# Performance work log

Hardware: AMD Instinct MI355X
Metric: run time of the kernel (lower is better)

The kernel has to match this reference:

```python
import jax, jax.numpy as jnp
import numpy as np

B, N, H, T = 128, 512, 128, 32


def setup_inputs() -> dict:
    key = jax.random.key(0)
    ks = jax.random.split(key, 6)
    s = 0.05  # small init scale keeps softmax logits sane
    return {
        "encoder_outputs": jax.random.normal(ks[0], (B, N, H), jnp.float32),
        "W_ih": jax.random.normal(ks[1], (4 * H, H), jnp.float32) * s,
        "W_hh": jax.random.normal(ks[2], (4 * H, H), jnp.float32) * s,
        "b_ih": jnp.zeros((4 * H,), jnp.float32),
        "b_hh": jnp.zeros((4 * H,), jnp.float32),
        "W1": jax.random.normal(ks[3], (H, H), jnp.float32) * s,
        "W2": jax.random.normal(ks[4], (H, H), jnp.float32) * s,
        "v": jax.random.normal(ks[5], (H,), jnp.float32) * s,
        "decode_steps": T,
    }


def reference(encoder_outputs, W_ih, W_hh, b_ih, b_hh, W1, W2, v, decode_steps):
    b, n, h = encoder_outputs.shape
    dtype = encoder_outputs.dtype
    # W1(encoder_outputs) is loop-invariant: hoist it (same math as the torch loop)
    enc_trans = jnp.einsum("bnh,kh->bnk", encoder_outputs, W1)  # [B,n,H]

    dec0 = encoder_outputs.mean(axis=1)  # [B,H]
    hx0 = jnp.zeros((b, h), dtype)
    cx0 = jnp.zeros((b, h), dtype)
    mask0 = jnp.zeros((b, n), bool)
    key0 = jax.random.key(42)
    rows = jnp.arange(b)

    def step(carry, _):
        dec_input, hx, cx, mask, key = carry
        # torch.nn.LSTMCell: gates ordered i, f, g, o
        gates = dec_input @ W_ih.T + b_ih + hx @ W_hh.T + b_hh  # [B,4H]
        i, f, g, o = jnp.split(gates, 4, axis=-1)
        i = jax.nn.sigmoid(i)
        f = jax.nn.sigmoid(f)
        g = jnp.tanh(g)
        o = jax.nn.sigmoid(o)
        cx_new = f * cx + i * g
        hx_new = o * jnp.tanh(cx_new)
        # additive attention scores
        dec_trans = hx_new @ W2.T  # [B,H]
        scores = jnp.einsum("bnh,h->bn", jnp.tanh(enc_trans + dec_trans[:, None, :]), v)
        scores = jnp.where(mask, -jnp.inf, scores)  # masked_fill(-inf)
        # sample next node (torch.multinomial on softmax == categorical on logits)
        key, sub = jax.random.split(key)
        idx = jax.random.categorical(sub, scores, axis=-1)  # [B]
        probs = jax.nn.softmax(scores, axis=-1)
        sel_log_prob = jnp.log(jnp.take_along_axis(probs, idx[:, None], axis=1)[:, 0] + 1e-9)
        mask_new = mask.at[rows, idx].set(True)
        dec_next = jnp.take_along_axis(encoder_outputs, idx[:, None, None], axis=1)[:, 0]  # [B,H]
        return (dec_next, hx_new, cx_new, mask_new, key), (idx, sel_log_prob)

    _, (tours, log_probs) = jax.lax.scan(
        step, (dec0, hx0, cx0, mask0, key0), xs=None, length=decode_steps
    )
    return tours.T, log_probs.T  # [B,T], [B,T]
```

## Files before the change

kernel.cpp:

```cpp
#include <hip/hip_runtime.h>
#include <cstdint>
#include <cstddef>


constexpr int B = 128, N = 512, H = 128, T = 32;
constexpr int G4 = 4 * H;
constexpr float TINYF = 1.17549435e-38f;

__host__ __device__ inline uint32_t rotl32(uint32_t v, int d) {
  return (v << d) | (v >> (32 - d));
}

__host__ __device__ inline void tf2x32(uint32_t k0, uint32_t k1,
                                       uint32_t x0, uint32_t x1,
                                       uint32_t& o0, uint32_t& o1) {
  uint32_t ks2 = k0 ^ k1 ^ 0x1BD11BDAu;
  x0 += k0; x1 += k1;
#define TF_R(r) x0 += x1; x1 = rotl32(x1, (r)); x1 ^= x0;
  TF_R(13) TF_R(15) TF_R(26) TF_R(6)
  x0 += k1; x1 += ks2 + 1u;
  TF_R(17) TF_R(29) TF_R(16) TF_R(24)
  x0 += ks2; x1 += k0 + 2u;
  TF_R(13) TF_R(15) TF_R(26) TF_R(6)
  x0 += k0; x1 += k1 + 3u;
  TF_R(17) TF_R(29) TF_R(16) TF_R(24)
  x0 += k1; x1 += ks2 + 4u;
  TF_R(13) TF_R(15) TF_R(26) TF_R(6)
  x0 += ks2; x1 += k0 + 5u;
#undef TF_R
  o0 = x0; o1 = x1;
}

struct KeyArgs { uint32_t k[2 * T]; };

static KeyArgs make_subkeys() {
  KeyArgs ka;
  uint32_t k0 = 0u, k1 = 42u;
  for (int t = 0; t < T; ++t) {
    uint32_t n0, n1, s0, s1;
    tf2x32(k0, k1, 0u, 0u, n0, n1);
    tf2x32(k0, k1, 0u, 1u, s0, s1);
    ka.k[2 * t] = s0; ka.k[2 * t + 1] = s1;
    k0 = n0; k1 = n1;
  }
  return ka;
}

__device__ inline uint32_t gumbel_bits(uint32_t sk0, uint32_t sk1, int i) {
  uint32_t o0, o1;
  tf2x32(sk0, sk1, 0u, (uint32_t)i, o0, o1);
  return o0 ^ o1;
}

__device__ inline float fast_tanh(float x) {
  float cx = fminf(9.0f, fmaxf(-9.0f, x));
  float t = __expf(2.0f * cx);
  return (t - 1.0f) * __builtin_amdgcn_rcpf(t + 1.0f);
}

__global__ void k_transpose(const float* __restrict__ Wih, const float* __restrict__ Whh,
                            const float* __restrict__ W2, const float* __restrict__ W1,
                            float* __restrict__ WihT, float* __restrict__ WhhT,
                            float* __restrict__ W2T, float* __restrict__ W1T) {
  int i = blockIdx.x * blockDim.x + threadIdx.x;
  if (i < H * G4) {
    int h = i >> 9, j = i & (G4 - 1);
    WihT[i] = Wih[j * H + h];
  } else if (i < 2 * H * G4) {
    int q = i - H * G4; int h = q >> 9, j = q & (G4 - 1);
    WhhT[q] = Whh[j * H + h];
  } else if (i < 2 * H * G4 + H * H) {
    int q = i - 2 * H * G4; int h = q >> 7, k = q & (H - 1);
    W2T[q] = W2[k * H + h];
  } else if (i < 2 * H * G4 + 2 * H * H) {
    int q = i - 2 * H * G4 - H * H; int h = q >> 7, k = q & (H - 1);
    W1T[q] = W1[k * H + h];
  }
}

__global__ __launch_bounds__(256) void k_enc_trans(const float* __restrict__ enc,
                                                   const float* __restrict__ W1T,
                                                   float* __restrict__ encT2) {
  __shared__ __align__(16) float es[16 * 128];
  int blk = blockIdx.x;
  int b = blk >> 5;
  int n0 = (blk & 31) << 4;
  const float* src = enc + ((size_t)b * N + n0) * H;
  for (int i = threadIdx.x; i < 16 * 128; i += 256) es[i] = src[i];
  __syncthreads();
  int k = threadIdx.x & 127, ng = threadIdx.x >> 7;
  float acc[8] = {0.f, 0.f, 0.f, 0.f, 0.f, 0.f, 0.f, 0.f};
  for (int h = 0; h < H; h += 4) {
    float w0 = W1T[(h + 0) * H + k];
    float w1 = W1T[(h + 1) * H + k];
    float w2 = W1T[(h + 2) * H + k];
    float w3 = W1T[(h + 3) * H + k];
#pragma unroll
    for (int j = 0; j < 8; ++j) {
      const float4 e = *(const float4*)&es[(ng * 8 + j) * 128 + h];
      acc[j] += w0 * e.x + w1 * e.y + w2 * e.z + w3 * e.w;
    }
  }
  float* dst = encT2 + (size_t)b * H * N + (size_t)k * N + n0 + ng * 8;
  ((float4*)dst)[0] = make_float4(acc[0], acc[1], acc[2], acc[3]);
  ((float4*)dst)[1] = make_float4(acc[4], acc[5], acc[6], acc[7]);
}

__global__ __launch_bounds__(1024) void k_decode(
    const float* __restrict__ enc, const float* __restrict__ encT2,
    const float* __restrict__ WihT, const float* __restrict__ WhhT,
    const float* __restrict__ W2T,
    const float* __restrict__ bih, const float* __restrict__ bhh,
    const float* __restrict__ v,
    KeyArgs keys, float* __restrict__ out) {
  __shared__ __align__(16) float xs[H];
  __shared__ __align__(16) float hs[H];
  __shared__ __align__(16) float cs[H];
  __shared__ __align__(16) float dt[H];
  __shared__ __align__(16) float vv[H];
  __shared__ __align__(16) float bsum[G4];
  __shared__ float pg[2][G4];
  __shared__ float ps[2][N];
  __shared__ float pdt[4][H];
  __shared__ float sc[N];
  __shared__ float wr_z[8], wr_m[8], wr_s[8];
  __shared__ int wr_i[8];
  __shared__ float s_smax;
  __shared__ int s_idx;

  const int tid = threadIdx.x;
  const int b = blockIdx.x;
  const int lane = tid & 63;
  const int wave = tid >> 6;
  const int half = tid >> 9;
  const int id = tid & 511;

  if (tid < 512) {
    int h = tid & 127, part = tid >> 7;
    float s = 0.f;
    const float* p = enc + ((size_t)b * N + part * 128) * H + h;
#pragma unroll 8
    for (int n = 0; n < 128; ++n) s += p[(size_t)n * H];
    pdt[part][h] = s;
    bsum[tid] = bih[tid] + bhh[tid];
  }
  if (tid < 128) { hs[tid] = 0.f; cs[tid] = 0.f; vv[tid] = v[tid]; }
  __syncthreads();
  if (tid < 128)
    xs[tid] = (pdt[0][tid] + pdt[1][tid] + pdt[2][tid] + pdt[3][tid]) * (1.0f / N);
  bool masked = false;
  __syncthreads();

  for (int t = 0; t < T; ++t) {
    {
      const float* wi = WihT + (size_t)(half * 64) * G4 + id;
      const float* wh = WhhT + (size_t)(half * 64) * G4 + id;
      const int hb = half * 64;
      float a0 = 0.f, a1 = 0.f;
#pragma unroll 8
      for (int h = 0; h < 64; ++h) {
        a0 += wi[h * G4] * xs[hb + h];
        a1 += wh[h * G4] * hs[hb + h];
      }
      pg[half][id] = a0 + a1;
    }
    __syncthreads();
    if (tid < 128) {
      float gi = pg[0][tid] + pg[1][tid] + bsum[tid];
      float gf = pg[0][H + tid] + pg[1][H + tid] + bsum[H + tid];
      float gg = pg[0][2 * H + tid] + pg[1][2 * H + tid] + bsum[2 * H + tid];
      float go = pg[0][3 * H + tid] + pg[1][3 * H + tid] + bsum[3 * H + tid];
      gi = 1.0f / (1.0f + expf(-gi));
      gf = 1.0f / (1.0f + expf(-gf));
      gg = tanhf(gg);
      go = 1.0f / (1.0f + expf(-go));
      float c = gf * cs[tid] + gi * gg;
      cs[tid] = c;
      hs[tid] = go * tanhf(c);
    }
    __syncthreads();
    if (tid < 512) {
      int k = tid & 127, part = tid >> 7;
      const float* w2 = W2T + (size_t)(part * 32) * H + k;
      const int hb = part * 32;
      float a = 0.f;
#pragma unroll 8
      for (int h = 0; h < 32; ++h) a += w2[h * H] * hs[hb + h];
      pdt[part][k] = a;
    }
    __syncthreads();
    if (tid < 128) dt[tid] = pdt[0][tid] + pdt[1][tid] + pdt[2][tid] + pdt[3][tid];
    __syncthreads();
    {
      const int kb = half * 64;
      const float* ep = encT2 + (size_t)b * (H * N) + (size_t)kb * N + id;
      float a0 = 0.f, a1 = 0.f;
#pragma unroll 8
      for (int kk = 0; kk < 64; kk += 2) {
        float e0 = ep[(size_t)kk * N];
        float e1 = ep[(size_t)(kk + 1) * N];
        a0 += vv[kb + kk] * fast_tanh(e0 + dt[kb + kk]);
        a1 += vv[kb + kk + 1] * fast_tanh(e1 + dt[kb + kk + 1]);
      }
      ps[half][id] = a0 + a1;
    }
    __syncthreads();
    if (tid < 512) {
      float s = masked ? -INFINITY : (ps[0][tid] + ps[1][tid]);
      sc[tid] = s;
      uint32_t bits = gumbel_bits(keys.k[2 * t], keys.k[2 * t + 1], b * N + tid);
      float f = __uint_as_float((bits >> 9) | 0x3f800000u) - 1.0f;
      float u = fmaxf(TINYF, f + TINYF);
      float g = -logf(-logf(u));
      float z = s + g;
      int zi = tid;
      float m = s;
#pragma unroll
      for (int d = 32; d >= 1; d >>= 1) {
        float oz = __shfl_xor(z, d);
        int oi = __shfl_xor(zi, d);
        float om = __shfl_xor(m, d);
        if (oz > z || (oz == z && oi < zi)) { z = oz; zi = oi; }
        m = fmaxf(m, om);
      }
      if (lane == 0) { wr_z[wave] = z; wr_i[wave] = zi; wr_m[wave] = m; }
    }
    __syncthreads();
    if (tid == 0) {
      float bz = wr_z[0]; int bi = wr_i[0]; float bm = wr_m[0];
#pragma unroll
      for (int w = 1; w < 8; ++w) {
        if (wr_z[w] > bz || (wr_z[w] == bz && wr_i[w] < bi)) { bz = wr_z[w]; bi = wr_i[w]; }
        bm = fmaxf(bm, wr_m[w]);
      }
      s_idx = bi; s_smax = bm;
    }
    __syncthreads();
    if (tid < 512) {
      float e = expf(sc[tid] - s_smax);
#pragma unroll
      for (int d = 32; d >= 1; d >>= 1) e += __shfl_xor(e, d);
      if (lane == 0) wr_s[wave] = e;
      if (tid == s_idx) masked = true;
    } else if (tid < 640) {
      xs[tid - 512] = enc[((size_t)b * N + s_idx) * H + (tid - 512)];
    }
    __syncthreads();
    if (tid == 0) {
      float sum = wr_s[0] + wr_s[1] + wr_s[2] + wr_s[3]
                + wr_s[4] + wr_s[5] + wr_s[6] + wr_s[7];
      float p = expf(sc[s_idx] - s_smax) / sum;
      out[(size_t)b * T + t] = (float)s_idx;
      out[(size_t)B * T + (size_t)b * T + t] = logf(p + 1e-9f);
    }
    __syncthreads();
  }
}

extern "C" void kernel_launch(void* const* d_in, const int* in_sizes, int n_in,
                              void* d_out, int out_size, void* d_ws, size_t ws_size,
                              hipStream_t stream) {
  (void)in_sizes; (void)n_in; (void)out_size; (void)ws_size;
  const float* enc = (const float*)d_in[0];
  const float* Wih = (const float*)d_in[1];
  const float* Whh = (const float*)d_in[2];
  const float* bih = (const float*)d_in[3];
  const float* bhh = (const float*)d_in[4];
  const float* W1  = (const float*)d_in[5];
  const float* W2  = (const float*)d_in[6];
  const float* v   = (const float*)d_in[7];
  float* out = (float*)d_out;
  float* ws = (float*)d_ws;

  float* WihT  = ws;
  float* WhhT  = ws + 65536;
  float* W2T   = ws + 131072;
  float* W1T   = ws + 147456;
  float* encT2 = ws + 163840;

  KeyArgs keys = make_subkeys();

  k_transpose<<<640, 256, 0, stream>>>(Wih, Whh, W2, W1, WihT, WhhT, W2T, W1T);
  k_enc_trans<<<B * N / 16, 256, 0, stream>>>(enc, W1T, encT2);
  k_decode<<<B, 1024, 0, stream>>>(enc, encT2, WihT, WhhT, W2T, bih, bhh, v, keys, out);
}
```

Before: 615.5 us.

## Fuse setup kernels, cache enc_trans in registers, precompute Gumbel noise, drop max pass

Merges the weight transpose and enc_trans kernels into one launch, with W1 transposed into padded shared memory per block. The decode kernel now keeps each thread's 64 enc_trans values in registers across all steps, precomputes all Gumbel noise into shared memory up front, and packs x/h and dt/v into float2 arrays. The softmax max-subtraction pass is removed, which merges the argmax and sum reductions and drops two barriers per step; this relies on scores staying small enough that exp does not overflow. Outputs are buffered in shared memory and written once at the end. The 64-float register array and the larger shared footprint raise register and LDS pressure.

New measurement: 628.7 us. +2.1%, slower.

```diff
diff --git a/kernel.cpp b/kernel.cpp
--- a/kernel.cpp
+++ b/kernel.cpp
@@ -58,30 +58,33 @@
   return (t - 1.0f) * __builtin_amdgcn_rcpf(t + 1.0f);
 }
 
-__global__ void k_transpose(const float* __restrict__ Wih, const float* __restrict__ Whh,
-                            const float* __restrict__ W2, const float* __restrict__ W1,
-                            float* __restrict__ WihT, float* __restrict__ WhhT,
-                            float* __restrict__ W2T, float* __restrict__ W1T) {
-  int i = blockIdx.x * blockDim.x + threadIdx.x;
-  if (i < H * G4) {
-    int h = i >> 9, j = i & (G4 - 1);
-    WihT[i] = Wih[j * H + h];
-  } else if (i < 2 * H * G4) {
-    int q = i - H * G4; int h = q >> 9, j = q & (G4 - 1);
-    WhhT[q] = Whh[j * H + h];
-  } else if (i < 2 * H * G4 + H * H) {
-    int q = i - 2 * H * G4; int h = q >> 7, k = q & (H - 1);
-    W2T[q] = W2[k * H + h];
-  } else if (i < 2 * H * G4 + 2 * H * H) {
-    int q = i - 2 * H * G4 - H * H; int h = q >> 7, k = q & (H - 1);
-    W1T[q] = W1[k * H + h];
-  }
-}
-
-__global__ __launch_bounds__(256) void k_enc_trans(const float* __restrict__ enc,
-                                                   const float* __restrict__ W1T,
-                                                   float* __restrict__ encT2) {
+__global__ __launch_bounds__(256) void k_setup(
+    const float* __restrict__ enc, const float* __restrict__ W1,
+    const float* __restrict__ Wih, const float* __restrict__ Whh,
+    const float* __restrict__ W2,
+    float* __restrict__ encT2, float* __restrict__ WihT,
+    float* __restrict__ WhhT, float* __restrict__ W2T) {
+  __shared__ float w1t[128 * 129];
   __shared__ __align__(16) float es[16 * 128];
+
+  if (blockIdx.x >= 4096) {
+    int base = (blockIdx.x - 4096) * 256 + threadIdx.x;
+    const int stride = 64 * 256;
+    for (int i = base; i < H * G4; i += stride) {
+      int h = i >> 9, j = i & (G4 - 1);
+      WihT[i] = Wih[j * H + h];
+      WhhT[i] = Whh[j * H + h];
+    }
+    for (int i = base; i < H * H; i += stride) {
+      int h = i >> 7, k = i & (H - 1);
+      W2T[i] = W2[k * H + h];
+    }
+    return;
+  }
+  for (int i = threadIdx.x; i < H * H; i += 256) {
+    int k = i >> 7, h = i & 127;
+    w1t[h * 129 + k] = W1[i];
+  }
   int blk = blockIdx.x;
   int b = blk >> 5;
   int n0 = (blk & 31) << 4;
@@ -91,10 +94,10 @@
   int k = threadIdx.x & 127, ng = threadIdx.x >> 7;
   float acc[8] = {0.f, 0.f, 0.f, 0.f, 0.f, 0.f, 0.f, 0.f};
   for (int h = 0; h < H; h += 4) {
-    float w0 = W1T[(h + 0) * H + k];
-    float w1 = W1T[(h + 1) * H + k];
-    float w2 = W1T[(h + 2) * H + k];
-    float w3 = W1T[(h + 3) * H + k];
+    float w0 = w1t[(h + 0) * 129 + k];
+    float w1 = w1t[(h + 1) * 129 + k];
+    float w2 = w1t[(h + 2) * 129 + k];
+    float w3 = w1t[(h + 3) * 129 + k];
 #pragma unroll
     for (int j = 0; j < 8; ++j) {
       const float4 e = *(const float4*)&es[(ng * 8 + j) * 128 + h];
@@ -106,34 +109,32 @@
   ((float4*)dst)[1] = make_float4(acc[4], acc[5], acc[6], acc[7]);
 }
 
-__global__ __launch_bounds__(1024) void k_decode(
+__global__ __launch_bounds__(1024, 4) void k_decode(
     const float* __restrict__ enc, const float* __restrict__ encT2,
     const float* __restrict__ WihT, const float* __restrict__ WhhT,
     const float* __restrict__ W2T,
     const float* __restrict__ bih, const float* __restrict__ bhh,
     const float* __restrict__ v,
     KeyArgs keys, float* __restrict__ out) {
-  __shared__ __align__(16) float xs[H];
-  __shared__ __align__(16) float hs[H];
-  __shared__ __align__(16) float cs[H];
-  __shared__ __align__(16) float dt[H];
-  __shared__ __align__(16) float vv[H];
+  __shared__ float2 xh[H];
+  __shared__ float cs[H];
+  __shared__ float2 dv[H];
   __shared__ __align__(16) float bsum[G4];
   __shared__ float pg[2][G4];
+  __shared__ float pdt[4][H];
   __shared__ float ps[2][N];
-  __shared__ float pdt[4][H];
   __shared__ float sc[N];
-  __shared__ float wr_z[8], wr_m[8], wr_s[8];
+  __shared__ float gb[T * N];
+  __shared__ float wr_z[8], wr_s[8];
   __shared__ int wr_i[8];
-  __shared__ float s_smax;
-  __shared__ int s_idx;
+  __shared__ float outb[2][T];
 
   const int tid = threadIdx.x;
   const int b = blockIdx.x;
   const int lane = tid & 63;
   const int wave = tid >> 6;
-  const int half = tid >> 9;
-  const int id = tid & 511;
+  const int kh = tid >> 9;
+  const int nn = tid & 511;
 
   if (tid < 512) {
     int h = tid & 127, part = tid >> 7;
@@ -144,25 +145,42 @@
     pdt[part][h] = s;
     bsum[tid] = bih[tid] + bhh[tid];
   }
-  if (tid < 128) { hs[tid] = 0.f; cs[tid] = 0.f; vv[tid] = v[tid]; }
+#pragma unroll
+  for (int q = 0; q < 16; ++q) {
+    int idx = q * 1024 + tid;
+    int tt = idx >> 9, n = idx & 511;
+    uint32_t bits = gumbel_bits(keys.k[2 * tt], keys.k[2 * tt + 1], b * N + n);
+    float f = __uint_as_float((bits >> 9) | 0x3f800000u) - 1.0f;
+    float u = fmaxf(TINYF, f + TINYF);
+    gb[tt * N + n] = -logf(-logf(u));
+  }
+  if (tid < 128) { cs[tid] = 0.f; dv[tid] = make_float2(0.f, v[tid]); }
+  float er[64];
+  {
+    const float* ep = encT2 + (size_t)b * (H * N) + (size_t)(kh * 64) * N + nn;
+#pragma unroll
+    for (int kk = 0; kk < 64; ++kk) er[kk] = ep[(size_t)kk * N];
+  }
   __syncthreads();
   if (tid < 128)
-    xs[tid] = (pdt[0][tid] + pdt[1][tid] + pdt[2][tid] + pdt[3][tid]) * (1.0f / N);
+    xh[tid] = make_float2(
+        (pdt[0][tid] + pdt[1][tid] + pdt[2][tid] + pdt[3][tid]) * (1.0f / N), 0.f);
   bool masked = false;
   __syncthreads();
 
   for (int t = 0; t < T; ++t) {
     {
-      const float* wi = WihT + (size_t)(half * 64) * G4 + id;
-      const float* wh = WhhT + (size_t)(half * 64) * G4 + id;
-      const int hb = half * 64;
+      const int hb = kh * 64;
+      const float* wi = WihT + (size_t)hb * G4 + nn;
+      const float* wh = WhhT + (size_t)hb * G4 + nn;
       float a0 = 0.f, a1 = 0.f;
 #pragma unroll 8
       for (int h = 0; h < 64; ++h) {
-        a0 += wi[h * G4] * xs[hb + h];
-        a1 += wh[h * G4] * hs[hb + h];
-      }
-      pg[half][id] = a0 + a1;
+        float2 xhv = xh[hb + h];
+        a0 += wi[h * G4] * xhv.x;
+        a1 += wh[h * G4] * xhv.y;
+      }
+      pg[kh][nn] = a0 + a1;
     }
     __syncthreads();
     if (tid < 128) {
@@ -176,7 +194,7 @@
       go = 1.0f / (1.0f + expf(-go));
       float c = gf * cs[tid] + gi * gg;
       cs[tid] = c;
-      hs[tid] = go * tanhf(c);
+      xh[tid].y = go * tanhf(c);
     }
     __syncthreads();
     if (tid < 512) {
@@ -185,75 +203,66 @@
       const int hb = part * 32;
       float a = 0.f;
 #pragma unroll 8
-      for (int h = 0; h < 32; ++h) a += w2[h * H] * hs[hb + h];
+      for (int h = 0; h < 32; ++h) a += w2[h * H] * xh[hb + h].y;
       pdt[part][k] = a;
     }
     __syncthreads();
-    if (tid < 128) dt[tid] = pdt[0][tid] + pdt[1][tid] + pdt[2][tid] + pdt[3][tid];
+    if (tid < 128)
+      dv[tid].x = pdt[0][tid] + pdt[1][tid] + pdt[2][tid] + pdt[3][tid];
     __syncthreads();
     {
-      const int kb = half * 64;
-      const float* ep = encT2 + (size_t)b * (H * N) + (size_t)kb * N + id;
+      const int kb = kh * 64;
       float a0 = 0.f, a1 = 0.f;
-#pragma unroll 8
+#pragma unroll
       for (int kk = 0; kk < 64; kk += 2) {
-        float e0 = ep[(size_t)kk * N];
-        float e1 = ep[(size_t)(kk + 1) * N];
-        a0 += vv[kb + kk] * fast_tanh(e0 + dt[kb + kk]);
-        a1 += vv[kb + kk + 1] * fast_tanh(e1 + dt[kb + kk + 1]);
-      }
-      ps[half][id] = a0 + a1;
+        float2 d0 = dv[kb + kk];
+        float2 d1 = dv[kb + kk + 1];
+        a0 += d0.y * fast_tanh(er[kk] + d0.x);
+        a1 += d1.y * fast_tanh(er[kk + 1] + d1.x);
+      }
+      ps[kh][nn] = a0 + a1;
     }
     __syncthreads();
     if (tid < 512) {
       float s = masked ? -INFINITY : (ps[0][tid] + ps[1][tid]);
       sc[tid] = s;
-      uint32_t bits = gumbel_bits(keys.k[2 * t], keys.k[2 * t + 1], b * N + tid);
-      float f = __uint_as_float((bits >> 9) | 0x3f800000u) - 1.0f;
-      float u = fmaxf(TINYF, f + TINYF);
-      float g = -logf(-logf(u));
-      float z = s + g;
+      float z = s + gb[t * N + tid];
       int zi = tid;
-      float m = s;
 #pragma unroll
       for (int d = 32; d >= 1; d >>= 1) {
         float oz = __shfl_xor(z, d);
         int oi = __shfl_xor(zi, d);
-        float om = __shfl_xor(m, d);
         if (oz > z || (oz == z && oi < zi)) { z = oz; zi = oi; }
-        m = fmaxf(m, om);
-      }
-      if (lane == 0) { wr_z[wave] = z; wr_i[wave] = zi; wr_m[wave] = m; }
-    }
-    __syncthreads();
-    if (tid == 0) {
-      float bz = wr_z[0]; int bi = wr_i[0]; float bm = wr_m[0];
+      }
+      float e = expf(s);
+#pragma unroll
+      for (int d = 32; d >= 1; d >>= 1) e += __shfl_xor(e, d);
+      if (lane == 0) { wr_z[wave] = z; wr_i[wave] = zi; wr_s[wave] = e; }
+    }
+    __syncthreads();
+    {
+      float bz = wr_z[0]; int bi = wr_i[0];
 #pragma unroll
       for (int w = 1; w < 8; ++w) {
-        if (wr_z[w] > bz || (wr_z[w] == bz && wr_i[w] < bi)) { bz = wr_z[w]; bi = wr_i[w]; }
-        bm = fmaxf(bm, wr_m[w]);
-      }
-      s_idx = bi; s_smax = bm;
-    }
-    __syncthreads();
-    if (tid < 512) {
-      float e = expf(sc[tid] - s_smax);
-#pragma unroll
-      for (int d = 32; d >= 1; d >>= 1) e += __shfl_xor(e, d);
-      if (lane == 0) wr_s[wave] = e;
-      if (tid == s_idx) masked = true;
-    } else if (tid < 640) {
-      xs[tid - 512] = enc[((size_t)b * N + s_idx) * H + (tid - 512)];
-    }
-    __syncthreads();
-    if (tid == 0) {
-      float sum = wr_s[0] + wr_s[1] + wr_s[2] + wr_s[3]
-                + wr_s[4] + wr_s[5] + wr_s[6] + wr_s[7];
-      float p = expf(sc[s_idx] - s_smax) / sum;
-      out[(size_t)b * T + t] = (float)s_idx;
-      out[(size_t)B * T + (size_t)b * T + t] = logf(p + 1e-9f);
-    }
-    __syncthreads();
+        float wz = wr_z[w]; int wj = wr_i[w];
+        if (wz > bz || (wz == bz && wj < bi)) { bz = wz; bi = wj; }
+      }
+      if (tid == bi) masked = true;
+      if (tid >= 512 && tid < 640)
+        xh[tid - 512].x = enc[((size_t)b * N + bi) * H + (tid - 512)];
+      if (tid == 0) {
+        float S = ((((((wr_s[0] + wr_s[1]) + wr_s[2]) + wr_s[3]) + wr_s[4])
+                    + wr_s[5]) + wr_s[6]) + wr_s[7];
+        float p = expf(sc[bi]) / S;
+        outb[0][t] = (float)bi;
+        outb[1][t] = logf(p + 1e-9f);
+      }
+    }
+    __syncthreads();
+  }
+  if (tid < T) {
+    out[(size_t)b * T + tid] = outb[0][tid];
+    out[(size_t)B * T + (size_t)b * T + tid] = outb[1][tid];
   }
 }
 
@@ -275,12 +284,11 @@
   float* WihT  = ws;
   float* WhhT  = ws + 65536;
   float* W2T   = ws + 131072;
-  float* W1T   = ws + 147456;
-  float* encT2 = ws + 163840;
+  float* encT2 = ws + 147456;
 
   KeyArgs keys = make_subkeys();
 
-  k_transpose<<<640, 256, 0, stream>>>(Wih, Whh, W2, W1, WihT, WhhT, W2T, W1T);
-  k_enc_trans<<<B * N / 16, 256, 0, stream>>>(enc, W1T, encT2);
-  k_decode<<<B, 1024, 0, stream>>>(enc, encT2, WihT, WhhT, W2T, bih, bhh, v, keys, out);
-}
+  k_setup<<<4160, 256, 0, stream>>>(enc, W1, Wih, Whh, W2, encT2, WihT, WhhT, W2T);
+  k_decode<<<B, 1024, 0, stream>>>(enc, encT2, WihT, WhhT, W2T, bih, bhh, v,
+                                   keys, out);
+}
```
